# Kernel tuning notes

Hardware: AMD Instinct MI355X
Metric: run time of the kernel (lower is better)

Reference implementation:

```python
import jax, jax.numpy as jnp
import numpy as np

B, C, RES, N_ANGLES = 32, 16, 128, 64


def setup_inputs() -> dict:
    key = jax.random.key(0)
    k1, k2, k3 = jax.random.split(key, 3)
    x = jax.random.normal(k1, (B, C, RES, RES), dtype=jnp.float32)
    # torch-radon setup: angles = np.linspace(0, 2*pi, 64)
    angles = jnp.linspace(0.0, 2.0 * np.pi, N_ANGLES).astype(jnp.float32)
    # Conv2d(16, 1, 1) params (kaiming-ish scale)
    conv_w = jax.random.normal(k2, (1, C, 1, 1), dtype=jnp.float32) * (1.0 / np.sqrt(C))
    conv_b = jax.random.normal(k3, (1,), dtype=jnp.float32) * 0.01
    return {"x": x, "angles": angles, "conv_w": conv_w, "conv_b": conv_b}


def _radon(x, angles):
    # x: (B, C, H, W) -> sinogram (B, C, n_angles, det_count)
    H = x.shape[-2]
    W = x.shape[-1]
    center = (H - 1) / 2.0
    # detector positions s and ray-integration positions t, in pixel units, centered
    coords = jnp.arange(H, dtype=jnp.float32) - center  # (RES,)

    def proj_one(carry, theta):
        c, s = jnp.cos(theta), jnp.sin(theta)
        # rotated sampling grid: (D, T) = (detector, along-ray)
        xs = coords[:, None] * c - coords[None, :] * s + center
        ys = coords[:, None] * s + coords[None, :] * c + center
        x0 = jnp.floor(xs)
        y0 = jnp.floor(ys)
        wx = xs - x0  # bilinear weights
        wy = ys - y0
        x0i = x0.astype(jnp.int32)
        y0i = y0.astype(jnp.int32)

        def g(yi, xi):
            # zero-padded gather: (B, C, D, T)
            valid = ((yi >= 0) & (yi < H) & (xi >= 0) & (xi < W)).astype(x.dtype)
            v = x[:, :, jnp.clip(yi, 0, H - 1), jnp.clip(xi, 0, W - 1)]
            return v * valid

        val = (g(y0i, x0i) * ((1.0 - wy) * (1.0 - wx))
               + g(y0i, x0i + 1) * ((1.0 - wy) * wx)
               + g(y0i + 1, x0i) * (wy * (1.0 - wx))
               + g(y0i + 1, x0i + 1) * (wy * wx))
        # line integral: sum along the ray (T axis) -> (B, C, D)
        return carry, val.sum(axis=-1)

    _, sino = jax.lax.scan(proj_one, 0, angles)  # (A, B, C, D)
    return jnp.transpose(sino, (1, 2, 0, 3))      # (B, C, A, D)


def reference(x, angles, conv_w, conv_b):
    sino = _radon(x, angles)  # (B, C, A, D)
    # 1x1 conv: contract channel dim
    out = jnp.einsum('bcad,oc->boad', sino, conv_w[:, :, 0, 0])
    return out + conv_b[None, :, None, None]
```

## Files before the change

kernel.cpp:

```cpp
#include <hip/hip_runtime.h>


#define B_    32
#define C_    16
#define RES   128
#define NA    64
#define SLDS  133
#define ROWS  132
#define NELEM (ROWS * SLDS)
#define NPADE 18432
#define NPAIR 16

typedef _Float16 half2v __attribute__((ext_vector_type(2)));

__global__ __launch_bounds__(256) void chanpack(const float* __restrict__ x,
                                                const float* __restrict__ w,
                                                unsigned int* __restrict__ pk) {
    const int blk = blockIdx.x;
    const int p   = blk >> 7;
    const int q   = blk & 127;
    const int t   = threadIdx.x;
    const int u   = t >> 7;
    const int m   = t & 127;

    __shared__ float rowbuf[2][128];

    float wr[C_];
#pragma unroll
    for (int c = 0; c < C_; ++c) wr[c] = w[c];

    const float* xb = x + ((size_t)(2 * p + u) * C_) * (RES * RES) + q * RES + m;
    float acc = 0.f;
#pragma unroll
    for (int c = 0; c < C_; ++c) acc = fmaf(wr[c], xb[c * (RES * RES)], acc);

    rowbuf[u][m] = acc;
    __syncthreads();

    unsigned int* dst = pk + (size_t)p * NPADE + (q + 2) * SLDS;
    if (t < SLDS) {
        int c = t;
        unsigned int v = 0u;
        if (c >= 2 && c <= 129)
            v = __builtin_bit_cast(unsigned int,
                    __builtin_amdgcn_cvt_pkrtz(rowbuf[0][c - 2], rowbuf[1][c - 2]));
        dst[c] = v;
    }

    if (q == 0) {
        unsigned int* base = pk + (size_t)p * NPADE;
        for (int k = t; k < 2 * SLDS; k += 256) {
            base[k] = 0u;
            base[130 * SLDS + k] = 0u;
        }
        for (int k = t; k < NPADE - NELEM; k += 256)
            base[NELEM + k] = 0u;
    }
}

__global__ __launch_bounds__(512, 2) void radon_k(const unsigned int* __restrict__ pk,
                                                  const float* __restrict__ angles,
                                                  const float* __restrict__ bias,
                                                  float* __restrict__ out) {
    __shared__ unsigned int lds[NPADE];
    const int bid = blockIdx.x;
    const int h   = bid & 1;
    const int grp = (bid >> 1) & 15;
    const int p   = bid >> 5;
    const int t   = threadIdx.x;

    {
        const uint4* src = (const uint4*)(pk + (size_t)p * NPADE);
        uint4*       dst = (uint4*)lds;
#pragma unroll
        for (int k = 0; k < 9; ++k) dst[k * 512 + t] = src[k * 512 + t];
    }
    __syncthreads();

    const int a = (t >> 7) * 16 + grp;
    const int i = t & 127;
    float th = angles[a];
    float s, c;
    __sincosf(th, &s, &c);

    const float ci = (float)i - 63.5f;
    const float j0 = (float)(h * 64);
    const float Xb = fmaf(ci, c, fmaf(63.5f - j0, s, 65.5f));
    const float Yb = fmaf(ci, s, fmaf(j0 - 63.5f, c, 65.5f));
    const float ns = -s;

    float acc0 = 0.f, acc1 = 0.f;
#pragma unroll 8
    for (int j = 0; j < 64; ++j) {
        float jf = (float)j;
        float X  = fmaf(jf, ns, Xb);
        float Y  = fmaf(jf, c,  Yb);
        float fx = floorf(X), fy = floorf(Y);
        float wx = X - fx,    wy = Y - fy;
        float gx = fminf(fmaxf(fx, 0.f), 130.f);
        float gy = fminf(fmaxf(fy, 0.f), 130.f);
        int addr = (int)fmaf(gy, (float)SLDS, gx);
        half2v q00 = __builtin_bit_cast(half2v, lds[addr]);
        half2v q01 = __builtin_bit_cast(half2v, lds[addr + 1]);
        half2v q10 = __builtin_bit_cast(half2v, lds[addr + SLDS]);
        half2v q11 = __builtin_bit_cast(half2v, lds[addr + SLDS + 1]);
        float un = 1.f - wx;
        float A0 = 1.f - wy;
        float w00 = A0 * un, w01 = A0 * wx, w10 = wy * un, w11 = wy * wx;
        acc0 = fmaf((float)q00.x, w00, acc0);
        acc1 = fmaf((float)q00.y, w00, acc1);
        acc0 = fmaf((float)q01.x, w01, acc0);
        acc1 = fmaf((float)q01.y, w01, acc1);
        acc0 = fmaf((float)q10.x, w10, acc0);
        acc1 = fmaf((float)q10.y, w10, acc1);
        acc0 = fmaf((float)q11.x, w11, acc0);
        acc1 = fmaf((float)q11.y, w11, acc1);
    }

    float bv = (h == 0) ? bias[0] : 0.f;
    atomicAdd(&out[(2 * p)     * (NA * RES) + a * RES + i], acc0 + bv);
    atomicAdd(&out[(2 * p + 1) * (NA * RES) + a * RES + i], acc1 + bv);
}

extern "C" void kernel_launch(void* const* d_in, const int* in_sizes, int n_in,
                              void* d_out, int out_size, void* d_ws, size_t ws_size,
                              hipStream_t stream) {
    const float* x      = (const float*)d_in[0];
    const float* angles = (const float*)d_in[1];
    const float* w      = (const float*)d_in[2];
    const float* bias   = (const float*)d_in[3];
    float* out = (float*)d_out;

    unsigned int* pk = (unsigned int*)d_ws;

    hipMemsetAsync(out, 0, (size_t)out_size * sizeof(float), stream);
    chanpack<<<dim3(NPAIR * RES), dim3(256), 0, stream>>>(x, w, pk);
    radon_k<<<dim3(NPAIR * 16 * 2), dim3(512), 0, stream>>>(pk, angles, bias, out);
}
```

Baseline: 97.71 us.

## Exploit angle symmetry by packing vertically flipped image to serve mirrored angles

The packed image now also stores a vertically flipped copy in each element, so one LDS gather serves both angle a and its mirror 63-a. The angle grid is symmetric under linspace(0, 2π), which lets each thread accumulate four outputs (two batches × two angles) per sample, halving the number of blocks and coordinate computations. In exchange, LDS usage doubles to 147 KB per block, occupancy drops (launch bound of 2 removed), and correctness depends on the flip mapping matching the mirrored angle geometry exactly.

```diff
diff --git a/kernel.cpp b/kernel.cpp
--- a/kernel.cpp
+++ b/kernel.cpp
@@ -15,7 +15,7 @@
 
 __global__ __launch_bounds__(256) void chanpack(const float* __restrict__ x,
                                                 const float* __restrict__ w,
-                                                unsigned int* __restrict__ pk) {
+                                                unsigned short* __restrict__ pk16) {
     const int blk = blockIdx.x;
     const int p   = blk >> 7;
     const int q   = blk & 127;
@@ -37,49 +37,55 @@
     rowbuf[u][m] = acc;
     __syncthreads();
 
-    unsigned int* dst = pk + (size_t)p * NPADE + (q + 2) * SLDS;
     if (t < SLDS) {
         int c = t;
-        unsigned int v = 0u;
-        if (c >= 2 && c <= 129)
-            v = __builtin_bit_cast(unsigned int,
-                    __builtin_amdgcn_cvt_pkrtz(rowbuf[0][c - 2], rowbuf[1][c - 2]));
-        dst[c] = v;
+        unsigned short v0 = 0, v1 = 0;
+        if (c >= 2 && c <= 129) {
+            v0 = __builtin_bit_cast(unsigned short, (_Float16)rowbuf[0][c - 2]);
+            v1 = __builtin_bit_cast(unsigned short, (_Float16)rowbuf[1][c - 2]);
+        }
+        size_t base = (size_t)p * NPADE * 4;
+        size_t e1 = base + (size_t)((q + 2)   * SLDS + c) * 4;
+        size_t e2 = base + (size_t)((129 - q) * SLDS + c) * 4;
+        pk16[e1 + 0] = v0;  pk16[e1 + 2] = v1;
+        pk16[e2 + 1] = v0;  pk16[e2 + 3] = v1;
     }
 
     if (q == 0) {
-        unsigned int* base = pk + (size_t)p * NPADE;
+        uint2* base = (uint2*)pk16 + (size_t)p * NPADE;
+        const uint2 z = make_uint2(0u, 0u);
         for (int k = t; k < 2 * SLDS; k += 256) {
-            base[k] = 0u;
-            base[130 * SLDS + k] = 0u;
+            base[k] = z;
+            base[130 * SLDS + k] = z;
         }
         for (int k = t; k < NPADE - NELEM; k += 256)
-            base[NELEM + k] = 0u;
+            base[NELEM + k] = z;
     }
 }
 
-__global__ __launch_bounds__(512, 2) void radon_k(const unsigned int* __restrict__ pk,
-                                                  const float* __restrict__ angles,
-                                                  const float* __restrict__ bias,
-                                                  float* __restrict__ out) {
-    __shared__ unsigned int lds[NPADE];
+__global__ __launch_bounds__(512) void radon_k(const uint2* __restrict__ pk,
+                                               const float* __restrict__ angles,
+                                               const float* __restrict__ bias,
+                                               float* __restrict__ out) {
+    __shared__ uint2 lds[NPADE];
     const int bid = blockIdx.x;
     const int h   = bid & 1;
-    const int grp = (bid >> 1) & 15;
-    const int p   = bid >> 5;
+    const int ag  = (bid >> 1) & 7;
+    const int p   = bid >> 4;
     const int t   = threadIdx.x;
 
     {
         const uint4* src = (const uint4*)(pk + (size_t)p * NPADE);
         uint4*       dst = (uint4*)lds;
 #pragma unroll
-        for (int k = 0; k < 9; ++k) dst[k * 512 + t] = src[k * 512 + t];
+        for (int k = 0; k < 18; ++k) dst[k * 512 + t] = src[k * 512 + t];
     }
     __syncthreads();
 
-    const int a = (t >> 7) * 16 + grp;
-    const int i = t & 127;
-    float th = angles[a];
+    const int ap = (t >> 7) * 8 + ag;
+    const int a1 = ap, a2 = 63 - ap;
+    const int i  = t & 127;
+    float th = angles[a1];
     float s, c;
     __sincosf(th, &s, &c);
 
@@ -89,7 +95,7 @@
     const float Yb = fmaf(ci, s, fmaf(j0 - 63.5f, c, 65.5f));
     const float ns = -s;
 
-    float acc0 = 0.f, acc1 = 0.f;
+    float ab0a1 = 0.f, ab0a2 = 0.f, ab1a1 = 0.f, ab1a2 = 0.f;
 #pragma unroll 8
     for (int j = 0; j < 64; ++j) {
         float jf = (float)j;
@@ -100,26 +106,44 @@
         float gx = fminf(fmaxf(fx, 0.f), 130.f);
         float gy = fminf(fmaxf(fy, 0.f), 130.f);
         int addr = (int)fmaf(gy, (float)SLDS, gx);
-        half2v q00 = __builtin_bit_cast(half2v, lds[addr]);
-        half2v q01 = __builtin_bit_cast(half2v, lds[addr + 1]);
-        half2v q10 = __builtin_bit_cast(half2v, lds[addr + SLDS]);
-        half2v q11 = __builtin_bit_cast(half2v, lds[addr + SLDS + 1]);
+        uint2 q00 = lds[addr];
+        uint2 q01 = lds[addr + 1];
+        uint2 q10 = lds[addr + SLDS];
+        uint2 q11 = lds[addr + SLDS + 1];
         float un = 1.f - wx;
         float A0 = 1.f - wy;
         float w00 = A0 * un, w01 = A0 * wx, w10 = wy * un, w11 = wy * wx;
-        acc0 = fmaf((float)q00.x, w00, acc0);
-        acc1 = fmaf((float)q00.y, w00, acc1);
-        acc0 = fmaf((float)q01.x, w01, acc0);
-        acc1 = fmaf((float)q01.y, w01, acc1);
-        acc0 = fmaf((float)q10.x, w10, acc0);
-        acc1 = fmaf((float)q10.y, w10, acc1);
-        acc0 = fmaf((float)q11.x, w11, acc0);
-        acc1 = fmaf((float)q11.y, w11, acc1);
+
+        half2v e00a = __builtin_bit_cast(half2v, q00.x), e00b = __builtin_bit_cast(half2v, q00.y);
+        half2v e01a = __builtin_bit_cast(half2v, q01.x), e01b = __builtin_bit_cast(half2v, q01.y);
+        half2v e10a = __builtin_bit_cast(half2v, q10.x), e10b = __builtin_bit_cast(half2v, q10.y);
+        half2v e11a = __builtin_bit_cast(half2v, q11.x), e11b = __builtin_bit_cast(half2v, q11.y);
+
+        ab0a1 = fmaf((float)e00a.x, w00, ab0a1);
+        ab0a2 = fmaf((float)e00a.y, w00, ab0a2);
+        ab1a1 = fmaf((float)e00b.x, w00, ab1a1);
+        ab1a2 = fmaf((float)e00b.y, w00, ab1a2);
+        ab0a1 = fmaf((float)e01a.x, w01, ab0a1);
+        ab0a2 = fmaf((float)e01a.y, w01, ab0a2);
+        ab1a1 = fmaf((float)e01b.x, w01, ab1a1);
+        ab1a2 = fmaf((float)e01b.y, w01, ab1a2);
+        ab0a1 = fmaf((float)e10a.x, w10, ab0a1);
+        ab0a2 = fmaf((float)e10a.y, w10, ab0a2);
+        ab1a1 = fmaf((float)e10b.x, w10, ab1a1);
+        ab1a2 = fmaf((float)e10b.y, w10, ab1a2);
+        ab0a1 = fmaf((float)e11a.x, w11, ab0a1);
+        ab0a2 = fmaf((float)e11a.y, w11, ab0a2);
+        ab1a1 = fmaf((float)e11b.x, w11, ab1a1);
+        ab1a2 = fmaf((float)e11b.y, w11, ab1a2);
     }
 
     float bv = (h == 0) ? bias[0] : 0.f;
-    atomicAdd(&out[(2 * p)     * (NA * RES) + a * RES + i], acc0 + bv);
-    atomicAdd(&out[(2 * p + 1) * (NA * RES) + a * RES + i], acc1 + bv);
+    float* o0 = out + (size_t)(2 * p) * (NA * RES);
+    float* o1 = o0 + NA * RES;
+    atomicAdd(&o0[a1 * RES + i], ab0a1 + bv);
+    atomicAdd(&o0[a2 * RES + i], ab0a2 + bv);
+    atomicAdd(&o1[a1 * RES + i], ab1a1 + bv);
+    atomicAdd(&o1[a2 * RES + i], ab1a2 + bv);
 }
 
 extern "C" void kernel_launch(void* const* d_in, const int* in_sizes, int n_in,
@@ -131,9 +155,10 @@
     const float* bias   = (const float*)d_in[3];
     float* out = (float*)d_out;
 
-    unsigned int* pk = (unsigned int*)d_ws;
+    unsigned short* pk16 = (unsigned short*)d_ws;
 
     hipMemsetAsync(out, 0, (size_t)out_size * sizeof(float), stream);
-    chanpack<<<dim3(NPAIR * RES), dim3(256), 0, stream>>>(x, w, pk);
-    radon_k<<<dim3(NPAIR * 16 * 2), dim3(512), 0, stream>>>(pk, angles, bias, out);
+    chanpack<<<dim3(NPAIR * RES), dim3(256), 0, stream>>>(x, w, pk16);
+    radon_k<<<dim3(NPAIR * 8 * 2), dim3(512), 0, stream>>>((const uint2*)pk16,
+                                                           angles, bias, out);
 }
```

Result: no change. 98.18 us (+0.5%).
